# Kernel tuning notes

Hardware: AMD Instinct MI355X
Metric: run time of the kernel (lower is better)

The kernel has to match this reference:

```python
import jax, jax.numpy as jnp
import numpy as np

NUM_EXPERT = 8
IN_FEAT = 1024
OUT_FEAT = 1024
N_TOKENS = 8192


def setup_inputs() -> dict:
    key = jax.random.key(0)
    k_inp, k_gate, k_w = jax.random.split(key, 3)
    inp = jax.random.normal(k_inp, (N_TOKENS, IN_FEAT), dtype=jnp.float32)
    gate = jax.random.randint(k_gate, (N_TOKENS,), 0, NUM_EXPERT, dtype=jnp.int32)
    # FMoELinear weight: [num_expert, out_feat, in_feat], kaiming-uniform-like init
    bound = 1.0 / np.sqrt(IN_FEAT)
    weight = jax.random.uniform(
        k_w, (NUM_EXPERT, OUT_FEAT, IN_FEAT), dtype=jnp.float32,
        minval=-bound, maxval=bound)
    return {"inp": inp, "gate": gate, "weight": weight}


def reference(inp, gate, weight):
    # out[i] = weight[gate[i]] @ inp[i]  (top-1 MoE dispatch + grouped GEMM + combine)
    # Loop over the small fixed expert set via scan; each step does a masked
    # dense GEMM so only tokens routed to expert e contribute.
    n, _ = inp.shape
    num_expert, out_feat, _ = weight.shape

    def body(acc, ew):
        e, w_e = ew  # w_e: [out_feat, in_feat]
        mask = (gate == e).astype(inp.dtype)[:, None]  # [n, 1]
        acc = acc + (inp * mask) @ w_e.T               # [n, out_feat]
        return acc, None

    init = jnp.zeros((n, out_feat), dtype=inp.dtype)
    out, _ = jax.lax.scan(body, init, (jnp.arange(num_expert), weight))
    return out
```

## Files before the change

kernel.cpp:

```cpp
#include <hip/hip_runtime.h>
#include <hip/hip_bf16.h>

#define N_TOKENS 8192
#define IN_FEAT 1024
#define OUT_FEAT 1024
#define NUM_EXPERT 8

#define BM 128
#define BN 128
#define BK 32
#define LDSW 20

typedef __bf16 bf16x8 __attribute__((ext_vector_type(8)));
typedef float f32x4 __attribute__((ext_vector_type(4)));

__device__ __forceinline__ unsigned int rne16(float x) {
    union { float f; unsigned int u; } c;
    c.f = x;
    unsigned int u = c.u;
    u += 0x7fffu + ((u >> 16) & 1u);
    return u >> 16;
}
__device__ __forceinline__ unsigned int pk2(float x, float y) {
    return rne16(x) | (rne16(y) << 16);
}

__global__ __launch_bounds__(1024) void moe_sort(const int* __restrict__ gate,
                                                 int* __restrict__ perm,
                                                 int* __restrict__ seg) {
    __shared__ int cnt[NUM_EXPERT];
    __shared__ int cur[NUM_EXPERT];
    const int t = threadIdx.x;
    const int lane = t & 63;
    const unsigned long long lt = (lane == 0) ? 0ull : (~0ull >> (64 - lane));

    if (t < NUM_EXPERT) cnt[t] = 0;
    __syncthreads();

    for (int i = t; i < N_TOKENS; i += 1024) {
        int g = gate[i];
        #pragma unroll
        for (int e = 0; e < NUM_EXPERT; ++e) {
            unsigned long long m = __ballot(g == e);
            if (g == e && (m & lt) == 0ull) {
                atomicAdd(&cnt[e], __popcll(m));
            }
        }
    }
    __syncthreads();

    if (t == 0) {
        int s = 0;
        #pragma unroll
        for (int e = 0; e < NUM_EXPERT; ++e) { cur[e] = s; seg[e] = s; s += cnt[e]; }
        seg[NUM_EXPERT] = s;
    }
    __syncthreads();

    for (int i = t; i < N_TOKENS; i += 1024) {
        int g = gate[i];
        #pragma unroll
        for (int e = 0; e < NUM_EXPERT; ++e) {
            unsigned long long m = __ballot(g == e);
            if (g == e) {
                int rank = __popcll(m & lt);
                int leader = (int)__ffsll((unsigned long long)m) - 1;
                int p0 = 0;
                if (rank == 0) p0 = atomicAdd(&cur[e], __popcll(m));
                p0 = __shfl(p0, leader);
                perm[p0 + rank] = i;
            }
        }
    }
}

__global__ __launch_bounds__(256, 2) void moe_gemm(
    const float* __restrict__ inp,
    const float* __restrict__ weight,
    const int* __restrict__ perm,
    const int* __restrict__ seg,
    float* __restrict__ out) {

    const int bid = blockIdx.x;
    const int e = bid >> 9;
    const int rem = bid & 511;
    const int mtile = rem >> 3;
    const int ntile = rem & 7;

    const int base = seg[e];
    const int cnt = seg[e + 1] - base;
    if (mtile * BM >= cnt) return;

    __shared__ unsigned int lA[BM * LDSW];
    __shared__ unsigned int lB[BN * LDSW];
    __shared__ int rowids[BM];

    const int t = threadIdx.x;
    if (t < BM) {
        int r = mtile * BM + t;
        rowids[t] = (r < cnt) ? perm[base + r] : -1;
    }
    __syncthreads();

    const int srow = t >> 1;
    const int scol = (t & 1) << 4;
    const int tokA = rowids[srow];
    const bool aval = (tokA >= 0);
    const float* aptr = inp + (aval ? tokA : 0) * IN_FEAT + scol;
    const float* bptr = weight + e * (OUT_FEAT * IN_FEAT)
                        + (ntile * BN + srow) * IN_FEAT + scol;
    const int sdst = srow * LDSW + (scol >> 1);

    const int wave = t >> 6;
    const int lane = t & 63;
    const int wm = (wave & 1) << 6;
    const int wn = (wave >> 1) << 6;
    const int l15 = lane & 15;
    const int quad = lane >> 4;

    f32x4 acc[4][4];
    #pragma unroll
    for (int i = 0; i < 4; ++i)
        #pragma unroll
        for (int j = 0; j < 4; ++j)
            acc[i][j] = (f32x4)0.0f;

    float4 ra[4], rb[4];
    {
        const float4* ap = (const float4*)aptr;
        const float4* bp = (const float4*)bptr;
        #pragma unroll
        for (int i = 0; i < 4; ++i) { ra[i] = ap[i]; rb[i] = bp[i]; }
    }

    for (int k0 = 0; k0 < IN_FEAT; k0 += BK) {
        unsigned int ua[8], ub[8];
        #pragma unroll
        for (int i = 0; i < 4; ++i) {
            ua[2 * i]     = pk2(ra[i].x, ra[i].y);
            ua[2 * i + 1] = pk2(ra[i].z, ra[i].w);
            ub[2 * i]     = pk2(rb[i].x, rb[i].y);
            ub[2 * i + 1] = pk2(rb[i].z, rb[i].w);
        }
        if (!aval) {
            #pragma unroll
            for (int i = 0; i < 8; ++i) ua[i] = 0u;
        }

        __syncthreads();
        *(uint4*)&lA[sdst]     = make_uint4(ua[0], ua[1], ua[2], ua[3]);
        *(uint4*)&lA[sdst + 4] = make_uint4(ua[4], ua[5], ua[6], ua[7]);
        *(uint4*)&lB[sdst]     = make_uint4(ub[0], ub[1], ub[2], ub[3]);
        *(uint4*)&lB[sdst + 4] = make_uint4(ub[4], ub[5], ub[6], ub[7]);
        __syncthreads();

        if (k0 + BK < IN_FEAT) {
            const float4* ap = (const float4*)(aptr + k0 + BK);
            const float4* bp = (const float4*)(bptr + k0 + BK);
            #pragma unroll
            for (int i = 0; i < 4; ++i) { ra[i] = ap[i]; rb[i] = bp[i]; }
        }

        bf16x8 af[4], bq[4];
        #pragma unroll
        for (int i = 0; i < 4; ++i)
            af[i] = *(const bf16x8*)&lA[(wm + i * 16 + l15) * LDSW + (quad << 2)];
        #pragma unroll
        for (int i = 0; i < 4; ++i)
            bq[i] = *(const bf16x8*)&lB[(wn + i * 16 + l15) * LDSW + (quad << 2)];

        #pragma unroll
        for (int i = 0; i < 4; ++i)
            #pragma unroll
            for (int j = 0; j < 4; ++j)
                acc[i][j] = __builtin_amdgcn_mfma_f32_16x16x32_bf16(
                    af[i], bq[j], acc[i][j], 0, 0, 0);
    }

    #pragma unroll
    for (int mi = 0; mi < 4; ++mi) {
        #pragma unroll
        for (int r = 0; r < 4; ++r) {
            int row = wm + mi * 16 + quad * 4 + r;
            int token = rowids[row];
            if (token >= 0) {
                float* op = out + token * OUT_FEAT + ntile * BN + wn;
                #pragma unroll
                for (int ni = 0; ni < 4; ++ni)
                    op[ni * 16 + l15] = acc[mi][ni][r];
            }
        }
    }
}

extern "C" void kernel_launch(void* const* d_in, const int* in_sizes, int n_in,
                              void* d_out, int out_size, void* d_ws, size_t ws_size,
                              hipStream_t stream) {
    const float* inp = (const float*)d_in[0];
    const int* gate = (const int*)d_in[1];
    const float* weight = (const float*)d_in[2];
    float* out = (float*)d_out;

    int* perm = (int*)d_ws;
    int* seg = perm + N_TOKENS;

    moe_sort<<<1, 1024, 0, stream>>>(gate, perm, seg);

    const int grid = NUM_EXPERT * (N_TOKENS / BM) * (OUT_FEAT / BN);
    moe_gemm<<<grid, 256, 0, stream>>>(inp, weight, perm, seg, out);
}
```

Measured before the change: 174.8 us.

## Parallelize token sort across blocks and shrink GEMM N-tile to 64

Replaces the single-block sort with a multi-block histogram, a one-thread scan and a multi-block scatter, so routing uses many CUs instead of one. The GEMM tile narrows from 128 to 64 columns with a raised occupancy hint and a grid ordered m-tile major, giving more blocks and better spread across CUs. The trade-off is more launches plus a memset, a lower reuse ratio per tile, and token order inside each expert that is no longer deterministic.

```diff
diff --git a/kernel.cpp b/kernel.cpp
--- a/kernel.cpp
+++ b/kernel.cpp
@@ -7,7 +7,7 @@
 #define NUM_EXPERT 8
 
 #define BM 128
-#define BN 128
+#define BN 64
 #define BK 32
 #define LDSW 20
 
@@ -25,56 +25,50 @@
     return rne16(x) | (rne16(y) << 16);
 }
 
-__global__ __launch_bounds__(1024) void moe_sort(const int* __restrict__ gate,
-                                                 int* __restrict__ perm,
-                                                 int* __restrict__ seg) {
-    __shared__ int cnt[NUM_EXPERT];
-    __shared__ int cur[NUM_EXPERT];
+
+__global__ __launch_bounds__(256) void moe_hist(const int* __restrict__ gate,
+                                                int* __restrict__ cnt) {
+    __shared__ int lc[NUM_EXPERT];
+    const int t = threadIdx.x;
+    if (t < NUM_EXPERT) lc[t] = 0;
+    __syncthreads();
+    int g = gate[blockIdx.x * 256 + t];
+    atomicAdd(&lc[g], 1);
+    __syncthreads();
+    if (t < NUM_EXPERT) atomicAdd(&cnt[t], lc[t]);
+}
+
+__global__ void moe_scan(const int* __restrict__ cnt,
+                         int* __restrict__ seg, int* __restrict__ cur) {
+    int s = 0;
+    #pragma unroll
+    for (int e = 0; e < NUM_EXPERT; ++e) { seg[e] = s; cur[e] = s; s += cnt[e]; }
+    seg[NUM_EXPERT] = s;
+}
+
+__global__ __launch_bounds__(256) void moe_scatter(const int* __restrict__ gate,
+                                                   int* __restrict__ cur,
+                                                   int* __restrict__ perm) {
     const int t = threadIdx.x;
     const int lane = t & 63;
     const unsigned long long lt = (lane == 0) ? 0ull : (~0ull >> (64 - lane));
-
-    if (t < NUM_EXPERT) cnt[t] = 0;
-    __syncthreads();
-
-    for (int i = t; i < N_TOKENS; i += 1024) {
-        int g = gate[i];
-        #pragma unroll
-        for (int e = 0; e < NUM_EXPERT; ++e) {
-            unsigned long long m = __ballot(g == e);
-            if (g == e && (m & lt) == 0ull) {
-                atomicAdd(&cnt[e], __popcll(m));
-            }
-        }
-    }
-    __syncthreads();
-
-    if (t == 0) {
-        int s = 0;
-        #pragma unroll
-        for (int e = 0; e < NUM_EXPERT; ++e) { cur[e] = s; seg[e] = s; s += cnt[e]; }
-        seg[NUM_EXPERT] = s;
-    }
-    __syncthreads();
-
-    for (int i = t; i < N_TOKENS; i += 1024) {
-        int g = gate[i];
-        #pragma unroll
-        for (int e = 0; e < NUM_EXPERT; ++e) {
-            unsigned long long m = __ballot(g == e);
-            if (g == e) {
-                int rank = __popcll(m & lt);
-                int leader = (int)__ffsll((unsigned long long)m) - 1;
-                int p0 = 0;
-                if (rank == 0) p0 = atomicAdd(&cur[e], __popcll(m));
-                p0 = __shfl(p0, leader);
-                perm[p0 + rank] = i;
-            }
-        }
-    }
-}
-
-__global__ __launch_bounds__(256, 2) void moe_gemm(
+    const int i = blockIdx.x * 256 + t;
+    int g = gate[i];
+    #pragma unroll
+    for (int e = 0; e < NUM_EXPERT; ++e) {
+        unsigned long long m = __ballot(g == e);
+        if (g == e) {
+            int rank = __popcll(m & lt);
+            int leader = (int)__ffsll((unsigned long long)m) - 1;
+            int p0 = 0;
+            if (rank == 0) p0 = atomicAdd(&cur[e], __popcll(m));
+            p0 = __shfl(p0, leader);
+            perm[p0 + rank] = i;
+        }
+    }
+}
+
+__global__ __launch_bounds__(256, 4) void moe_gemm(
     const float* __restrict__ inp,
     const float* __restrict__ weight,
     const int* __restrict__ perm,
@@ -82,10 +76,9 @@
     float* __restrict__ out) {
 
     const int bid = blockIdx.x;
-    const int e = bid >> 9;
-    const int rem = bid & 511;
-    const int mtile = rem >> 3;
-    const int ntile = rem & 7;
+    const int mtile = bid >> 7;
+    const int e = (bid >> 4) & 7;
+    const int ntile = bid & 15;
 
     const int base = seg[e];
     const int cnt = seg[e + 1] - base;
@@ -107,38 +100,46 @@
     const int tokA = rowids[srow];
     const bool aval = (tokA >= 0);
     const float* aptr = inp + (aval ? tokA : 0) * IN_FEAT + scol;
+    const int sdstA = srow * LDSW + (scol >> 1);
+    const int browB = t >> 2;
+    const int bcol = (t & 3) << 3;
     const float* bptr = weight + e * (OUT_FEAT * IN_FEAT)
-                        + (ntile * BN + srow) * IN_FEAT + scol;
-    const int sdst = srow * LDSW + (scol >> 1);
+                        + (ntile * BN + browB) * IN_FEAT + bcol;
+    const int sdstB = browB * LDSW + (bcol >> 1);
 
     const int wave = t >> 6;
     const int lane = t & 63;
     const int wm = (wave & 1) << 6;
-    const int wn = (wave >> 1) << 6;
+    const int wn = (wave >> 1) << 5;
     const int l15 = lane & 15;
     const int quad = lane >> 4;
 
-    f32x4 acc[4][4];
+    f32x4 acc[4][2];
     #pragma unroll
     for (int i = 0; i < 4; ++i)
         #pragma unroll
-        for (int j = 0; j < 4; ++j)
+        for (int j = 0; j < 2; ++j)
             acc[i][j] = (f32x4)0.0f;
 
-    float4 ra[4], rb[4];
+    float4 ra[4], rb[2];
     {
         const float4* ap = (const float4*)aptr;
         const float4* bp = (const float4*)bptr;
         #pragma unroll
-        for (int i = 0; i < 4; ++i) { ra[i] = ap[i]; rb[i] = bp[i]; }
+        for (int i = 0; i < 4; ++i) ra[i] = ap[i];
+        #pragma unroll
+        for (int i = 0; i < 2; ++i) rb[i] = bp[i];
     }
 
     for (int k0 = 0; k0 < IN_FEAT; k0 += BK) {
-        unsigned int ua[8], ub[8];
+        unsigned int ua[8], ub[4];
         #pragma unroll
         for (int i = 0; i < 4; ++i) {
             ua[2 * i]     = pk2(ra[i].x, ra[i].y);
             ua[2 * i + 1] = pk2(ra[i].z, ra[i].w);
+        }
+        #pragma unroll
+        for (int i = 0; i < 2; ++i) {
             ub[2 * i]     = pk2(rb[i].x, rb[i].y);
             ub[2 * i + 1] = pk2(rb[i].z, rb[i].w);
         }
@@ -148,31 +149,32 @@
         }
 
         __syncthreads();
-        *(uint4*)&lA[sdst]     = make_uint4(ua[0], ua[1], ua[2], ua[3]);
-        *(uint4*)&lA[sdst + 4] = make_uint4(ua[4], ua[5], ua[6], ua[7]);
-        *(uint4*)&lB[sdst]     = make_uint4(ub[0], ub[1], ub[2], ub[3]);
-        *(uint4*)&lB[sdst + 4] = make_uint4(ub[4], ub[5], ub[6], ub[7]);
+        *(uint4*)&lA[sdstA]     = make_uint4(ua[0], ua[1], ua[2], ua[3]);
+        *(uint4*)&lA[sdstA + 4] = make_uint4(ua[4], ua[5], ua[6], ua[7]);
+        *(uint4*)&lB[sdstB]     = make_uint4(ub[0], ub[1], ub[2], ub[3]);
         __syncthreads();
 
         if (k0 + BK < IN_FEAT) {
             const float4* ap = (const float4*)(aptr + k0 + BK);
             const float4* bp = (const float4*)(bptr + k0 + BK);
             #pragma unroll
-            for (int i = 0; i < 4; ++i) { ra[i] = ap[i]; rb[i] = bp[i]; }
-        }
-
-        bf16x8 af[4], bq[4];
+            for (int i = 0; i < 4; ++i) ra[i] = ap[i];
+            #pragma unroll
+            for (int i = 0; i < 2; ++i) rb[i] = bp[i];
+        }
+
+        bf16x8 af[4], bq[2];
         #pragma unroll
         for (int i = 0; i < 4; ++i)
             af[i] = *(const bf16x8*)&lA[(wm + i * 16 + l15) * LDSW + (quad << 2)];
         #pragma unroll
+        for (int j = 0; j < 2; ++j)
+            bq[j] = *(const bf16x8*)&lB[(wn + j * 16 + l15) * LDSW + (quad << 2)];
+
+        #pragma unroll
         for (int i = 0; i < 4; ++i)
-            bq[i] = *(const bf16x8*)&lB[(wn + i * 16 + l15) * LDSW + (quad << 2)];
-
-        #pragma unroll
-        for (int i = 0; i < 4; ++i)
-            #pragma unroll
-            for (int j = 0; j < 4; ++j)
+            #pragma unroll
+            for (int j = 0; j < 2; ++j)
                 acc[i][j] = __builtin_amdgcn_mfma_f32_16x16x32_bf16(
                     af[i], bq[j], acc[i][j], 0, 0, 0);
     }
@@ -186,7 +188,7 @@
             if (token >= 0) {
                 float* op = out + token * OUT_FEAT + ntile * BN + wn;
                 #pragma unroll
-                for (int ni = 0; ni < 4; ++ni)
+                for (int ni = 0; ni < 2; ++ni)
                     op[ni * 16 + l15] = acc[mi][ni][r];
             }
         }
@@ -203,9 +205,14 @@
 
     int* perm = (int*)d_ws;
     int* seg = perm + N_TOKENS;
-
-    moe_sort<<<1, 1024, 0, stream>>>(gate, perm, seg);
-
-    const int grid = NUM_EXPERT * (N_TOKENS / BM) * (OUT_FEAT / BN);
+    int* cnt = seg + 16;
+    int* cur = cnt + 8;
+
+    hipMemsetAsync(cnt, 0, 16 * sizeof(int), stream);
+    moe_hist<<<N_TOKENS / 256, 256, 0, stream>>>(gate, cnt);
+    moe_scan<<<1, 1, 0, stream>>>(cnt, seg, cur);
+    moe_scatter<<<N_TOKENS / 256, 256, 0, stream>>>(gate, cur, perm);
+
+    const int grid = (N_TOKENS / BM) * NUM_EXPERT * (OUT_FEAT / BN);
     moe_gemm<<<grid, 256, 0, stream>>>(inp, weight, perm, seg, out);
 }
```

Measured after the change: 179.1 us. 2.5% more time.
